# Optimization experiments

Measured on AMD Instinct MI355X. Metric: run time of the kernel, lower is better.

## Reference

```python
import jax, jax.numpy as jnp
import numpy as np

KEY_DIM = 64
SCALE_PER_SEQ = 1.0 / np.sqrt(KEY_DIM).astype(np.float32)   # attn_scale_factor_per_seq default
SCALE_OVER_SEQS = 1.0 / np.sqrt(KEY_DIM).astype(np.float32) # attn_scale_factor_over_seqs default


def setup_inputs() -> dict:
    key = jax.random.key(0)
    ks = jax.random.split(key, 6)
    b, i, t, j, d = 8, 256, 64, 256, 256
    kd, vd = KEY_DIM, 64
    return {
        "input_seq": jax.random.normal(ks[0], (b, i, d), dtype=jnp.float32),
        "memory_x": jax.random.normal(ks[1], (b, t, j, d), dtype=jnp.float32),
        "memory_y": jax.random.normal(ks[2], (b, t, j, d), dtype=jnp.float32),
        "Wq": jax.random.normal(ks[3], (d, kd), dtype=jnp.float32) * (1.0 / np.sqrt(d)),
        "bq": jnp.zeros((kd,), dtype=jnp.float32),
        "Wk": jax.random.normal(ks[4], (d, kd), dtype=jnp.float32) * (1.0 / np.sqrt(d)),
        "bk": jnp.zeros((kd,), dtype=jnp.float32),
        "Wv": jax.random.normal(ks[5], (d, vd), dtype=jnp.float32) * (1.0 / np.sqrt(d)),
        "bv": jnp.zeros((vd,), dtype=jnp.float32),
    }


def reference(input_seq, memory_x, memory_y, Wq, bq, Wk, bk, Wv, bv):
    # Dense projections
    queries = input_seq @ Wq + bq            # [b, i, kd]
    keys = memory_x @ Wk + bk                # [b, t, j, kd]
    values = memory_y @ Wv + bv              # [b, t, j, vd]

    # Raw scores between every query and every token of every memory sequence
    attn_mat = jnp.einsum('bik,btjk->btij', queries, keys)  # [b, t, i, j]

    # Level 1: within-sequence attention (softmax over tokens j)
    per_seq_attn = jax.nn.softmax(SCALE_PER_SEQ * attn_mat, axis=-1)
    per_seq_retrieved = jnp.einsum('btij,btjk->btik', per_seq_attn, values)  # [b, t, i, vd]

    # Level 2: over-sequences attention (max over j, softmax over t)
    mem_seq_scores = jnp.max(attn_mat, axis=-1)                      # [b, t, i]
    mem_seq_attn = jax.nn.softmax(SCALE_OVER_SEQS * mem_seq_scores, axis=1)

    retrieved_mems = jnp.einsum('bti,btik->bik', mem_seq_attn, per_seq_retrieved)  # [b, i, vd]
    return retrieved_mems
```

## Files before the change

### kernel.cpp

```cpp
#include <hip/hip_runtime.h>
#include <hip/hip_bf16.h>

#define NB 8
#define NT 64
#define NI 256
#define NJ 256
#define ND 256
#define NKD 64
#define NVD 64
#define SCL 0.125f

typedef __attribute__((ext_vector_type(4))) float f32x4;
typedef __attribute__((ext_vector_type(8))) short bf16x8;
typedef __attribute__((ext_vector_type(4))) short bf16x4;
typedef __attribute__((ext_vector_type(4))) unsigned int uint32x4;

#define MFMA16(A, B, C) __builtin_amdgcn_mfma_f32_16x16x32_bf16((A), (B), (C), 0, 0, 0)

#define R2B 32768

__device__ __forceinline__ unsigned short f2bf(float x) {
  return __builtin_bit_cast(unsigned short, __float2bfloat16(x));
}
__device__ __forceinline__ float bf2f(unsigned short h) {
  return __builtin_bit_cast(float, (unsigned)h << 16);
}
__device__ __forceinline__ void split8(const float* __restrict__ x, bf16x8& hi, bf16x8& lo) {
  #pragma unroll
  for (int e = 0; e < 8; ++e) {
    unsigned short h = f2bf(x[e]);
    hi[e] = (short)h;
    lo[e] = (short)f2bf(x[e] - bf2f(h));
  }
}

__global__ __launch_bounds__(64) void k_prep_projq(
    const float* __restrict__ x, const float* __restrict__ Wq,
    const float* __restrict__ bq,
    const float* __restrict__ Wk, const float* __restrict__ Wv,
    unsigned short* __restrict__ Wkth, unsigned short* __restrict__ Wvth,
    unsigned short* __restrict__ Qh, unsigned short* __restrict__ Ql) {
  int lane = threadIdx.x;
  if (blockIdx.x < 256) {
    int t = blockIdx.x * 64 + lane;
    int d = t >> 6, kd = t & 63;
    Wkth[kd * 256 + d] = f2bf(Wk[t]);
    Wvth[kd * 256 + d] = f2bf(Wv[t]);
    return;
  }
  int row = blockIdx.x - 256;
  __shared__ __align__(16) float xs[ND];
  const float* xr = x + (size_t)row * ND;
  #pragma unroll
  for (int cc = 0; cc < 4; ++cc) xs[lane + 64 * cc] = xr[lane + 64 * cc];
  __syncthreads();
  float acc = bq[lane];
  #pragma unroll 4
  for (int d = 0; d < ND; ++d) acc = fmaf(xs[d], Wq[d * NKD + lane], acc);
  unsigned short h = f2bf(acc);
  Qh[(size_t)row * NKD + lane] = h;
  Ql[(size_t)row * NKD + lane] = f2bf(acc - bf2f(h));
}

__device__ __forceinline__ void stage_plane(
    char* dstb, const unsigned short* __restrict__ Wt, int tid) {
  #pragma unroll
  for (int it = 0; it < 4; ++it) {
    int qq = tid + it * 512;
    int r = qq >> 5, pb = qq & 31;
    uint4 v = *(const uint4*)((const char*)Wt + (size_t)qq * 16);
    *(uint4*)(dstb + r * 512 + ((pb ^ (r & 7)) << 4)) = v;
  }
}

__global__ __launch_bounds__(512, 4) void k_fused(
    const float* __restrict__ Xm, const float* __restrict__ Ym,
    const unsigned short* __restrict__ Wkth, const unsigned short* __restrict__ Wvth,
    const float* __restrict__ bk, const float* __restrict__ bv,
    const unsigned short* __restrict__ Qh, const unsigned short* __restrict__ Ql,
    unsigned short* __restrict__ R,
    float* __restrict__ Sc) {
  __shared__ __align__(16) char smemb[65536];
  int tid = threadIdx.x;
  int bt = blockIdx.x, b = bt >> 6;
  int w = tid >> 6, lane = tid & 63, c = lane & 15, g = lane >> 4;

  const float* xr0 = Xm + (size_t)bt * 65536 + (size_t)(w * 32 + c) * 256 + g * 8;
  const float* xr1 = xr0 + 16 * 256;
  const float* yr0 = Ym + (size_t)bt * 65536 + (size_t)(w * 32 + c) * 256 + g * 8;
  const float* yr1 = yr0 + 16 * 256;

  float4 xa0 = *(const float4*)(xr0),      xa1 = *(const float4*)(xr0 + 4);
  float4 xa2 = *(const float4*)(xr1),      xa3 = *(const float4*)(xr1 + 4);
  float4 xb0 = *(const float4*)(xr0 + 32), xb1 = *(const float4*)(xr0 + 36);
  float4 xb2 = *(const float4*)(xr1 + 32), xb3 = *(const float4*)(xr1 + 36);
  float4 ya0 = *(const float4*)(yr0),      ya1 = *(const float4*)(yr0 + 4);
  float4 ya2 = *(const float4*)(yr1),      ya3 = *(const float4*)(yr1 + 4);
  float4 yb0 = *(const float4*)(yr0 + 32), yb1 = *(const float4*)(yr0 + 36);
  float4 yb2 = *(const float4*)(yr1 + 32), yb3 = *(const float4*)(yr1 + 36);

  stage_plane(smemb, Wkth, tid);
  stage_plane(smemb + R2B, Wvth, tid);
  __syncthreads();

  f32x4 kacc[4][2];
  f32x4 vacc[2][4];
  #pragma unroll
  for (int mf = 0; mf < 4; ++mf) { kacc[mf][0] = (f32x4)0.f; kacc[mf][1] = (f32x4)0.f; }
  #pragma unroll
  for (int mf = 0; mf < 2; ++mf)
    #pragma unroll
    for (int nf = 0; nf < 4; ++nf) vacc[mf][nf] = (f32x4)0.f;

  #pragma unroll
  for (int ks = 0; ks < 8; ++ks) {
    float x0[8], x1[8];
    if (ks & 1) {
      *(float4*)&x0[0] = xb0; *(float4*)&x0[4] = xb1;
      *(float4*)&x1[0] = xb2; *(float4*)&x1[4] = xb3;
      if (ks < 6) {
        xb0 = *(const float4*)(xr0 + (ks + 2) * 32);
        xb1 = *(const float4*)(xr0 + (ks + 2) * 32 + 4);
        xb2 = *(const float4*)(xr1 + (ks + 2) * 32);
        xb3 = *(const float4*)(xr1 + (ks + 2) * 32 + 4);
      }
    } else {
      *(float4*)&x0[0] = xa0; *(float4*)&x0[4] = xa1;
      *(float4*)&x1[0] = xa2; *(float4*)&x1[4] = xa3;
      if (ks < 6) {
        xa0 = *(const float4*)(xr0 + (ks + 2) * 32);
        xa1 = *(const float4*)(xr0 + (ks + 2) * 32 + 4);
        xa2 = *(const float4*)(xr1 + (ks + 2) * 32);
        xa3 = *(const float4*)(xr1 + (ks + 2) * 32 + 4);
      }
    }
    {
      bf16x8 b0h, b0l, b1h, b1l;
      split8(x0, b0h, b0l);
      split8(x1, b1h, b1l);
      #pragma unroll
      for (int mf = 0; mf < 4; ++mf) {
        int r = mf * 16 + c;
        int ba = r * 512 + (((ks * 4 + g) ^ (r & 7)) << 4);
        bf16x8 awh = *(const bf16x8*)(smemb + ba);
        kacc[mf][0] = MFMA16(awh, b0h, kacc[mf][0]);
        kacc[mf][0] = MFMA16(awh, b0l, kacc[mf][0]);
        kacc[mf][1] = MFMA16(awh, b1h, kacc[mf][1]);
        kacc[mf][1] = MFMA16(awh, b1l, kacc[mf][1]);
      }
    }
    float y0[8], y1[8];
    if (ks & 1) {
      *(float4*)&y0[0] = yb0; *(float4*)&y0[4] = yb1;
      *(float4*)&y1[0] = yb2; *(float4*)&y1[4] = yb3;
      if (ks < 6) {
        yb0 = *(const float4*)(yr0 + (ks + 2) * 32);
        yb1 = *(const float4*)(yr0 + (ks + 2) * 32 + 4);
        yb2 = *(const float4*)(yr1 + (ks + 2) * 32);
        yb3 = *(const float4*)(yr1 + (ks + 2) * 32 + 4);
      }
    } else {
      *(float4*)&y0[0] = ya0; *(float4*)&y0[4] = ya1;
      *(float4*)&y1[0] = ya2; *(float4*)&y1[4] = ya3;
      if (ks < 6) {
        ya0 = *(const float4*)(yr0 + (ks + 2) * 32);
        ya1 = *(const float4*)(yr0 + (ks + 2) * 32 + 4);
        ya2 = *(const float4*)(yr1 + (ks + 2) * 32);
        ya3 = *(const float4*)(yr1 + (ks + 2) * 32 + 4);
      }
    }
    {
      bf16x8 a0h, a0l, a1h, a1l;
      split8(y0, a0h, a0l);
      split8(y1, a1h, a1l);
      #pragma unroll
      for (int nf = 0; nf < 4; ++nf) {
        int r = nf * 16 + c;
        int ba = R2B + r * 512 + (((ks * 4 + g) ^ (r & 7)) << 4);
        bf16x8 bwh = *(const bf16x8*)(smemb + ba);
        vacc[0][nf] = MFMA16(a0h, bwh, vacc[0][nf]);
        vacc[0][nf] = MFMA16(a0l, bwh, vacc[0][nf]);
        vacc[1][nf] = MFMA16(a1h, bwh, vacc[1][nf]);
        vacc[1][nf] = MFMA16(a1l, bwh, vacc[1][nf]);
      }
    }
  }
  bf16x8 qbh[2][2], qbl[2][2];
  #pragma unroll
  for (int ks = 0; ks < 2; ++ks)
    #pragma unroll
    for (int ic = 0; ic < 2; ++ic) {
      size_t qo = ((size_t)b * NI + w * 32 + ic * 16 + c) * NKD + ks * 32 + g * 8;
      qbh[ks][ic] = *(const bf16x8*)(Qh + qo);
      qbl[ks][ic] = *(const bf16x8*)(Ql + qo);
    }
  __syncthreads();

  #pragma unroll
  for (int nf = 0; nf < 2; ++nf) {
    int j = w * 32 + nf * 16 + c;
    #pragma unroll
    for (int mf = 0; mf < 4; ++mf) {
      bf16x4 ph;
      #pragma unroll
      for (int r = 0; r < 4; ++r)
        ph[r] = (short)f2bf(kacc[mf][nf][r] + bk[mf * 16 + g * 4 + r]);
      int pb = mf * 2 + (g >> 1);
      int ba = j * 128 + ((pb ^ (j & 7)) << 4) + (g & 1) * 8;
      *(bf16x4*)(smemb + ba) = ph;
    }
  }
  #pragma unroll
  for (int nf = 0; nf < 4; ++nf) {
    int vd = nf * 16 + c;
    float bs = bv[vd];
    #pragma unroll
    for (int mf = 0; mf < 2; ++mf) {
      bf16x4 ph;
      #pragma unroll
      for (int r = 0; r < 4; ++r) ph[r] = (short)f2bf(vacc[mf][nf][r] + bs);
      int pb = w * 4 + mf * 2 + (g >> 1);
      int ba = R2B + vd * 512 + ((pb ^ (vd & 7)) << 4) + (g & 1) * 8;
      *(bf16x4*)(smemb + ba) = ph;
    }
  }
  __syncthreads();

  #pragma unroll
  for (int ic = 0; ic < 2; ++ic) {
    int i = w * 32 + ic * 16 + c;

    f32x4 sa[16];
    #pragma unroll
    for (int jf = 0; jf < 16; ++jf) sa[jf] = (f32x4)0.f;
    #pragma unroll
    for (int jf = 0; jf < 16; ++jf) {
      int j = jf * 16 + c;
      #pragma unroll
      for (int ks = 0; ks < 2; ++ks) {
        int ba = j * 128 + (((ks * 4 + g) ^ (j & 7)) << 4);
        bf16x8 kh = *(const bf16x8*)(smemb + ba);
        sa[jf] = MFMA16(kh, qbh[ks][ic], sa[jf]);
        sa[jf] = MFMA16(kh, qbl[ks][ic], sa[jf]);
      }
    }

    float mx = sa[0][0];
    #pragma unroll
    for (int jf = 0; jf < 16; ++jf)
      #pragma unroll
      for (int r = 0; r < 4; ++r) mx = fmaxf(mx, sa[jf][r]);
    mx = fmaxf(mx, __shfl_xor(mx, 16));
    mx = fmaxf(mx, __shfl_xor(mx, 32));
    if (g == 0) Sc[(size_t)bt * NI + i] = mx;
    float sum = 0.f;
    #pragma unroll
    for (int jf = 0; jf < 16; ++jf)
      #pragma unroll
      for (int r = 0; r < 4; ++r) {
        float p = __expf((sa[jf][r] - mx) * SCL);
        sa[jf][r] = p;
        sum += p;
      }
    sum += __shfl_xor(sum, 16);
    sum += __shfl_xor(sum, 32);
    float linv = 1.0f / sum;

    unsigned int plo[16], phi[16];
    #pragma unroll
    for (int jf = 0; jf < 16; ++jf) {
      plo[jf] = (unsigned int)f2bf(sa[jf][0]) | ((unsigned int)f2bf(sa[jf][1]) << 16);
      phi[jf] = (unsigned int)f2bf(sa[jf][2]) | ((unsigned int)f2bf(sa[jf][3]) << 16);
    }

    int srcA = c + 32 * (g & 1);
    int srcB = srcA + 16;
    bool hiH = (g >= 2);

    f32x4 racc[4];
    #pragma unroll
    for (int vf = 0; vf < 4; ++vf) racc[vf] = (f32x4)0.f;
    #pragma unroll
    for (int js = 0; js < 8; ++js) {
      int a0 = __shfl((int)plo[2 * js], srcA);
      int a1 = __shfl((int)phi[2 * js], srcA);
      int a2 = __shfl((int)plo[2 * js], srcB);
      int a3 = __shfl((int)phi[2 * js], srcB);
      int b0 = __shfl((int)plo[2 * js + 1], srcA);
      int b1 = __shfl((int)phi[2 * js + 1], srcA);
      int b2 = __shfl((int)plo[2 * js + 1], srcB);
      int b3 = __shfl((int)phi[2 * js + 1], srcB);
      uint32x4 pw;
      pw[0] = (unsigned int)(hiH ? b0 : a0);
      pw[1] = (unsigned int)(hiH ? b1 : a1);
      pw[2] = (unsigned int)(hiH ? b2 : a2);
      pw[3] = (unsigned int)(hiH ? b3 : a3);
      bf16x8 pf = __builtin_bit_cast(bf16x8, pw);
      #pragma unroll
      for (int vf = 0; vf < 4; ++vf) {
        int vd = vf * 16 + c;
        int vba = R2B + vd * 512 + (((js * 4 + g) ^ (vd & 7)) << 4);
        bf16x8 vh = *(const bf16x8*)(smemb + vba);
        racc[vf] = MFMA16(vh, pf, racc[vf]);
      }
    }

    #pragma unroll
    for (int vf = 0; vf < 4; ++vf) {
      bf16x4 rk;
      #pragma unroll
      for (int r = 0; r < 4; ++r) rk[r] = (short)f2bf(racc[vf][r] * linv);
      *(bf16x4*)(R + ((size_t)bt * NI + i) * NKD + vf * 16 + g * 4) = rk;
    }
  }
}

__global__ __launch_bounds__(256) void k_level2(
    const float* __restrict__ Sc,
    const unsigned short* __restrict__ R,
    float* __restrict__ out) {
  int w = threadIdx.x >> 6, lane = threadIdx.x & 63;
  int bi = blockIdx.x * 4 + w;
  int b = bi >> 8, i = bi & 255;
  float sc = Sc[((size_t)b * NT + lane) * NI + i];
  float mx = sc;
  #pragma unroll
  for (int off = 32; off; off >>= 1) mx = fmaxf(mx, __shfl_xor(mx, off));
  float e = __expf((sc - mx) * SCL);
  float sum = e;
  #pragma unroll
  for (int off = 32; off; off >>= 1) sum += __shfl_xor(sum, off);
  float wn = e / sum;
  float acc = 0.f;
  for (int t = 0; t < NT; ++t) {
    float wt = __shfl(wn, t);
    acc = fmaf(wt, bf2f(R[(((size_t)b * NT + t) * NI + i) * NKD + lane]), acc);
  }
  out[((size_t)b * NI + i) * NVD + lane] = acc;
}

extern "C" void kernel_launch(void* const* d_in, const int* in_sizes, int n_in,
                              void* d_out, int out_size, void* d_ws, size_t ws_size,
                              hipStream_t stream) {
  const float* x   = (const float*)d_in[0];
  const float* mxp = (const float*)d_in[1];
  const float* myp = (const float*)d_in[2];
  const float* Wq  = (const float*)d_in[3];
  const float* bq  = (const float*)d_in[4];
  const float* Wk  = (const float*)d_in[5];
  const float* bk  = (const float*)d_in[6];
  const float* Wv  = (const float*)d_in[7];
  const float* bv  = (const float*)d_in[8];
  float* out = (float*)d_out;

  char* p = (char*)d_ws;
  auto alloc = [&](size_t bytes) { char* r = p; p += (bytes + 255) & ~(size_t)255; return r; };
  unsigned short* Qh   = (unsigned short*)alloc(2048 * 64 * 2);
  unsigned short* Ql   = (unsigned short*)alloc(2048 * 64 * 2);
  unsigned short* Rw   = (unsigned short*)alloc((size_t)131072 * 64 * 2);
  float*          Scw  = (float*)alloc((size_t)131072 * 4);
  unsigned short* Wkth = (unsigned short*)alloc(64 * 256 * 2);
  unsigned short* Wvth = (unsigned short*)alloc(64 * 256 * 2);

  hipLaunchKernelGGL(k_prep_projq, dim3(256 + NB * NI), dim3(64), 0, stream,
                     x, Wq, bq, Wk, Wv, Wkth, Wvth, Qh, Ql);
  hipLaunchKernelGGL(k_fused, dim3(NB * NT), dim3(512), 0, stream,
                     mxp, myp, Wkth, Wvth, bk, bv, Qh, Ql, Rw, Scw);
  hipLaunchKernelGGL(k_level2, dim3(512), dim3(256), 0, stream, Scw, Rw, out);
}
```

Before: 96.68 us.

## Drop Q low-precision split, restructure Q projection, add MFMA priority hints

Removes the bf16 hi/lo split of Q so the score MFMAs run once instead of twice, and drops the Ql buffer. The Q projection kernel is restructured to stage Wq and 16 rows of x in LDS per 256-thread block, replacing 2048 tiny blocks. s_setprio hints wrap the MFMA loops to favour matrix issue over other waves. Dropping the Q low part lowers score precision, which could affect accuracy tolerance.

```diff
diff --git a/kernel.cpp b/kernel.cpp
--- a/kernel.cpp
+++ b/kernel.cpp
@@ -34,32 +34,43 @@
   }
 }
 
-__global__ __launch_bounds__(64) void k_prep_projq(
+__global__ __launch_bounds__(256) void k_prep_projq(
     const float* __restrict__ x, const float* __restrict__ Wq,
     const float* __restrict__ bq,
     const float* __restrict__ Wk, const float* __restrict__ Wv,
     unsigned short* __restrict__ Wkth, unsigned short* __restrict__ Wvth,
-    unsigned short* __restrict__ Qh, unsigned short* __restrict__ Ql) {
-  int lane = threadIdx.x;
-  if (blockIdx.x < 256) {
-    int t = blockIdx.x * 64 + lane;
-    int d = t >> 6, kd = t & 63;
-    Wkth[kd * 256 + d] = f2bf(Wk[t]);
-    Wvth[kd * 256 + d] = f2bf(Wv[t]);
+    unsigned short* __restrict__ Qh) {
+  int tid = threadIdx.x;
+  if (blockIdx.x >= 128) {
+    int t0 = (blockIdx.x - 128) * 2048 + tid * 8;
+    #pragma unroll
+    for (int e = 0; e < 8; ++e) {
+      int t = t0 + e;
+      int d = t >> 6, kd = t & 63;
+      Wkth[kd * 256 + d] = f2bf(Wk[t]);
+      Wvth[kd * 256 + d] = f2bf(Wv[t]);
+    }
     return;
   }
-  int row = blockIdx.x - 256;
-  __shared__ __align__(16) float xs[ND];
-  const float* xr = x + (size_t)row * ND;
-  #pragma unroll
-  for (int cc = 0; cc < 4; ++cc) xs[lane + 64 * cc] = xr[lane + 64 * cc];
+  __shared__ __align__(16) float wqs[256 * 64];
+  __shared__ __align__(16) float xs[16 * 256];
+  #pragma unroll 8
+  for (int it = 0; it < 64; ++it)
+    wqs[tid + it * 256] = Wq[tid + it * 256];
+  int r0 = blockIdx.x * 16;
+  #pragma unroll
+  for (int it = 0; it < 16; ++it)
+    xs[tid + it * 256] = x[(size_t)r0 * 256 + tid + it * 256];
   __syncthreads();
-  float acc = bq[lane];
-  #pragma unroll 4
-  for (int d = 0; d < ND; ++d) acc = fmaf(xs[d], Wq[d * NKD + lane], acc);
-  unsigned short h = f2bf(acc);
-  Qh[(size_t)row * NKD + lane] = h;
-  Ql[(size_t)row * NKD + lane] = f2bf(acc - bf2f(h));
+  int kd = tid & 63, rr = tid >> 6;
+  #pragma unroll
+  for (int rp = 0; rp < 4; ++rp) {
+    int r = rp * 4 + rr;
+    float acc = bq[kd];
+    #pragma unroll 8
+    for (int d = 0; d < 256; ++d) acc = fmaf(xs[r * 256 + d], wqs[d * 64 + kd], acc);
+    Qh[(size_t)(r0 + r) * 64 + kd] = f2bf(acc);
+  }
 }
 
 __device__ __forceinline__ void stage_plane(
@@ -77,7 +88,7 @@
     const float* __restrict__ Xm, const float* __restrict__ Ym,
     const unsigned short* __restrict__ Wkth, const unsigned short* __restrict__ Wvth,
     const float* __restrict__ bk, const float* __restrict__ bv,
-    const unsigned short* __restrict__ Qh, const unsigned short* __restrict__ Ql,
+    const unsigned short* __restrict__ Qh,
     unsigned short* __restrict__ R,
     float* __restrict__ Sc) {
   __shared__ __align__(16) char smemb[65536];
@@ -138,6 +149,7 @@
       bf16x8 b0h, b0l, b1h, b1l;
       split8(x0, b0h, b0l);
       split8(x1, b1h, b1l);
+      __builtin_amdgcn_s_setprio(1);
       #pragma unroll
       for (int mf = 0; mf < 4; ++mf) {
         int r = mf * 16 + c;
@@ -148,6 +160,7 @@
         kacc[mf][1] = MFMA16(awh, b1h, kacc[mf][1]);
         kacc[mf][1] = MFMA16(awh, b1l, kacc[mf][1]);
       }
+      __builtin_amdgcn_s_setprio(0);
     }
     float y0[8], y1[8];
     if (ks & 1) {
@@ -173,6 +186,7 @@
       bf16x8 a0h, a0l, a1h, a1l;
       split8(y0, a0h, a0l);
       split8(y1, a1h, a1l);
+      __builtin_amdgcn_s_setprio(1);
       #pragma unroll
       for (int nf = 0; nf < 4; ++nf) {
         int r = nf * 16 + c;
@@ -183,16 +197,16 @@
         vacc[1][nf] = MFMA16(a1h, bwh, vacc[1][nf]);
         vacc[1][nf] = MFMA16(a1l, bwh, vacc[1][nf]);
       }
-    }
-  }
-  bf16x8 qbh[2][2], qbl[2][2];
+      __builtin_amdgcn_s_setprio(0);
+    }
+  }
+  bf16x8 qbh[2][2];
   #pragma unroll
   for (int ks = 0; ks < 2; ++ks)
     #pragma unroll
     for (int ic = 0; ic < 2; ++ic) {
       size_t qo = ((size_t)b * NI + w * 32 + ic * 16 + c) * NKD + ks * 32 + g * 8;
       qbh[ks][ic] = *(const bf16x8*)(Qh + qo);
-      qbl[ks][ic] = *(const bf16x8*)(Ql + qo);
     }
   __syncthreads();
 
@@ -233,6 +247,7 @@
     f32x4 sa[16];
     #pragma unroll
     for (int jf = 0; jf < 16; ++jf) sa[jf] = (f32x4)0.f;
+    __builtin_amdgcn_s_setprio(1);
     #pragma unroll
     for (int jf = 0; jf < 16; ++jf) {
       int j = jf * 16 + c;
@@ -241,9 +256,9 @@
         int ba = j * 128 + (((ks * 4 + g) ^ (j & 7)) << 4);
         bf16x8 kh = *(const bf16x8*)(smemb + ba);
         sa[jf] = MFMA16(kh, qbh[ks][ic], sa[jf]);
-        sa[jf] = MFMA16(kh, qbl[ks][ic], sa[jf]);
-      }
-    }
+      }
+    }
+    __builtin_amdgcn_s_setprio(0);
 
     float mx = sa[0][0];
     #pragma unroll
@@ -296,6 +311,7 @@
       pw[2] = (unsigned int)(hiH ? b2 : a2);
       pw[3] = (unsigned int)(hiH ? b3 : a3);
       bf16x8 pf = __builtin_bit_cast(bf16x8, pw);
+      __builtin_amdgcn_s_setprio(1);
       #pragma unroll
       for (int vf = 0; vf < 4; ++vf) {
         int vd = vf * 16 + c;
@@ -303,6 +319,7 @@
         bf16x8 vh = *(const bf16x8*)(smemb + vba);
         racc[vf] = MFMA16(vh, pf, racc[vf]);
       }
+      __builtin_amdgcn_s_setprio(0);
     }
 
     #pragma unroll
@@ -356,15 +373,14 @@
   char* p = (char*)d_ws;
   auto alloc = [&](size_t bytes) { char* r = p; p += (bytes + 255) & ~(size_t)255; return r; };
   unsigned short* Qh   = (unsigned short*)alloc(2048 * 64 * 2);
-  unsigned short* Ql   = (unsigned short*)alloc(2048 * 64 * 2);
   unsigned short* Rw   = (unsigned short*)alloc((size_t)131072 * 64 * 2);
   float*          Scw  = (float*)alloc((size_t)131072 * 4);
   unsigned short* Wkth = (unsigned short*)alloc(64 * 256 * 2);
   unsigned short* Wvth = (unsigned short*)alloc(64 * 256 * 2);
 
-  hipLaunchKernelGGL(k_prep_projq, dim3(256 + NB * NI), dim3(64), 0, stream,
-                     x, Wq, bq, Wk, Wv, Wkth, Wvth, Qh, Ql);
+  hipLaunchKernelGGL(k_prep_projq, dim3(136), dim3(256), 0, stream,
+                     x, Wq, bq, Wk, Wv, Wkth, Wvth, Qh);
   hipLaunchKernelGGL(k_fused, dim3(NB * NT), dim3(512), 0, stream,
-                     mxp, myp, Wkth, Wvth, bk, bv, Qh, Ql, Rw, Scw);
+                     mxp, myp, Wkth, Wvth, bk, bv, Qh, Rw, Scw);
   hipLaunchKernelGGL(k_level2, dim3(512), dim3(256), 0, stream, Scw, Rw, out);
 }
```

New measurement: 170.2 us. 76.0% more time.
